# Performance work log

Hardware: AMD Instinct MI355X
Metric: run time of the kernel (lower is better)

Reference implementation:

```python
import jax, jax.numpy as jnp
import numpy as np

OBS, ACT, HID, P, B = 128, 32, 256, 64, 4096
EPS = 1e-5


def _block(x, W, b, g, be, act=True):
    # x: [B, P, Din]; W: [P, Din, Dout]; b/g/be: [P, Dout]
    y = jnp.einsum('bpi,pio->bpo', x, W) + b
    # GroupNorm with one group per sub-policy: normalize over Dout per (b, p)
    mu = jnp.mean(y, axis=-1, keepdims=True)
    var = jnp.var(y, axis=-1, keepdims=True)
    y = (y - mu) * jax.lax.rsqrt(var + EPS) * g + be
    return jax.nn.elu(y) if act else y


def setup_inputs() -> dict:
    key = jax.random.key(0)
    ks = jax.random.split(key, 17)
    s = 0.05
    return {
        'observation': jax.random.normal(ks[0], (B, OBS), dtype=jnp.float32),
        'W1': jax.random.normal(ks[1], (P, OBS, HID), dtype=jnp.float32) * s,
        'b1': jax.random.normal(ks[2], (P, HID), dtype=jnp.float32) * s,
        'g1': jnp.ones((P, HID), dtype=jnp.float32),
        'be1': jnp.zeros((P, HID), dtype=jnp.float32),
        'W2': jax.random.normal(ks[3], (P, HID, HID), dtype=jnp.float32) * s,
        'b2': jax.random.normal(ks[4], (P, HID), dtype=jnp.float32) * s,
        'g2': jnp.ones((P, HID), dtype=jnp.float32),
        'be2': jnp.zeros((P, HID), dtype=jnp.float32),
        'W3': jax.random.normal(ks[5], (P, HID, HID), dtype=jnp.float32) * s,
        'b3': jax.random.normal(ks[6], (P, HID), dtype=jnp.float32) * s,
        'g3': jnp.ones((P, HID), dtype=jnp.float32),
        'be3': jnp.zeros((P, HID), dtype=jnp.float32),
        'W4': jax.random.normal(ks[7], (P, HID, ACT), dtype=jnp.float32) * s,
        'b4': jax.random.normal(ks[8], (P, ACT), dtype=jnp.float32) * s,
        'g4': jnp.ones((P, ACT), dtype=jnp.float32),
        'be4': jnp.zeros((P, ACT), dtype=jnp.float32),
    }


def reference(observation, W1, b1, g1, be1, W2, b2, g2, be2,
              W3, b3, g3, be3, W4, b4, g4, be4):
    # broadcast observation to each sub-policy: [B, P, OBS]
    x = jnp.broadcast_to(observation[:, None, :], (observation.shape[0], P, OBS))
    x = _block(x, W1, b1, g1, be1, act=True)
    x = _block(x, W2, b2, g2, be2, act=True)
    x = _block(x, W3, b3, g3, be3, act=True)
    x = _block(x, W4, b4, g4, be4, act=False)
    return x  # [B, P, ACT] action logits
```

## Files before the change

### kernel.cpp

```cpp
#include <hip/hip_runtime.h>

#define B_    4096
#define P_    64
#define OBS_  128
#define HID_  256
#define ACTD_ 32

typedef __attribute__((ext_vector_type(8)))  __bf16 bf16x8;
typedef __attribute__((ext_vector_type(2)))  __bf16 bf16x2_t;
typedef __attribute__((ext_vector_type(2)))  float  f32x2;
typedef __attribute__((ext_vector_type(4)))  float  f32x4;
typedef __attribute__((ext_vector_type(16))) float  f32x16;

#define XSTRIDE 264

#define WS1 0L
#define WS2 2097152L
#define WS3 6291456L
#define WS4 10485760L

#if defined(__has_builtin)
#if __has_builtin(__builtin_amdgcn_cvt_pk_bf16_f32)
#define HAVE_CVT_PK_BF16 1
#endif
#endif
#ifndef HAVE_CVT_PK_BF16
#define HAVE_CVT_PK_BF16 0
#endif

__device__ __forceinline__ unsigned short f2bf(float x) {
    unsigned u = __builtin_bit_cast(unsigned, x);
    u = (u + 0x7fffu + ((u >> 16) & 1u)) >> 16;
    return (unsigned short)u;
}

__device__ __forceinline__ unsigned pack_bf16_rne(float a, float b) {
#if HAVE_CVT_PK_BF16
    bf16x2_t p = __builtin_amdgcn_cvt_pk_bf16_f32(a, b);
    return __builtin_bit_cast(unsigned, p);
#else
    unsigned ua = __builtin_bit_cast(unsigned, a);
    unsigned ub = __builtin_bit_cast(unsigned, b);
    ua = ua + 0x7fffu + ((ua >> 16) & 1u);
    ub = ub + 0x7fffu + ((ub >> 16) & 1u);
    return __builtin_amdgcn_perm(ub, ua, 0x07060302u);
#endif
}

__device__ __forceinline__ void elu2_asm(float &a, float &b) {
    float ra, rb;
    asm volatile(
        "v_mul_f32 %0, 0x3fb8aa3b, %2\n\t"
        "v_mul_f32 %1, 0x3fb8aa3b, %3\n\t"
        "v_exp_f32 %0, %0\n\t"
        "v_exp_f32 %1, %1\n\t"
        "s_nop 0\n\t"
        "v_add_f32 %0, -1.0, %0\n\t"
        "v_add_f32 %1, -1.0, %1\n\t"
        "v_cmp_lt_f32 vcc, 0, %2\n\t"
        "v_cndmask_b32 %0, %0, %2, vcc\n\t"
        "v_cmp_lt_f32 vcc, 0, %3\n\t"
        "v_cndmask_b32 %1, %1, %3, vcc"
        : "=&v"(ra), "=&v"(rb) : "v"(a), "v"(b) : "vcc");
    a = ra; b = rb;
}

template<int K, int N>
__device__ __forceinline__ void prep_body(const float* __restrict__ W,
                                          unsigned short* __restrict__ out,
                                          int b, int t)
{
    constexpr int CH = K / 32;
    int tid  = b * 256 + t;
    int n    = tid % N;
    int rest = tid / N;
    int u    = rest % 4;
    rest    /= 4;
    int c    = rest % CH;
    int p    = rest / CH;
    const float* __restrict__ src = W + ((long)(p * K + c * 32 + u * 8)) * N + n;
    unsigned short tmp[8];
#pragma unroll
    for (int j = 0; j < 8; ++j)
        tmp[j] = f2bf(src[(long)j * N]);
    unsigned short* dst = out + ((((long)(p * CH + c) * 4 + u) * N + n) * 8);
    *reinterpret_cast<uint4*>(dst) = *reinterpret_cast<const uint4*>(tmp);
}

extern "C" __global__ __launch_bounds__(256)
void prep_all(const float* __restrict__ W1, const float* __restrict__ W2,
              const float* __restrict__ W3, const float* __restrict__ W4,
              unsigned short* __restrict__ ws)
{
    int b = blockIdx.x, t = threadIdx.x;
    if      (b < 1024) prep_body<128, 256>(W1, ws + WS1, b,        t);
    else if (b < 3072) prep_body<256, 256>(W2, ws + WS2, b - 1024, t);
    else if (b < 5120) prep_body<256, 256>(W3, ws + WS3, b - 3072, t);
    else               prep_body<256, 32 >(W4, ws + WS4, b - 5120, t);
}

template<int KCH>
__device__ __forceinline__ void layer256(
    unsigned short* __restrict__ X,
    const char* __restrict__ wsrc,
    const float* __restrict__ bp, const float* __restrict__ gp, const float* __restrict__ bep,
    float2* __restrict__ part, float2* __restrict__ stats,
    int tid, bool elu)
{
    const int w  = tid >> 6;
    const int l5 = tid & 31;
    const int h  = (tid & 63) >> 5;

    const bf16x8* __restrict__ Wp = (const bf16x8*)wsrc + (h * 256 + w * 64 + l5);
    const int nb = w * 64 + 4 * h;

    f32x16 acc[2][2];
#pragma unroll
    for (int nt = 0; nt < 2; ++nt)
#pragma unroll
        for (int q = 0; q < 4; ++q) {
            const float4 b4 = *reinterpret_cast<const float4*>(bp + nb + nt * 32 + 8 * q);
#pragma unroll
            for (int mt = 0; mt < 2; ++mt) {
                acc[nt][mt][4 * q + 0] = b4.x;
                acc[nt][mt][4 * q + 1] = b4.y;
                acc[nt][mt][4 * q + 2] = b4.z;
                acc[nt][mt][4 * q + 3] = b4.w;
            }
        }

    bf16x8 wb0[4], wb1[4];
#pragma unroll
    for (int i = 0; i < 4; ++i) {
        wb0[i] = Wp[i * 512];
        wb1[i] = Wp[i * 512 + 32];
    }
#pragma unroll
    for (int c = 0; c < KCH; ++c) {
        const int k0 = c * 16 + h * 8;
        const bf16x8 w0 = wb0[c & 3];
        const bf16x8 w1 = wb1[c & 3];
        if (c + 4 < KCH) {
            wb0[c & 3] = Wp[(c + 4) * 512];
            wb1[c & 3] = Wp[(c + 4) * 512 + 32];
        }
        bf16x8 x0 = *(const bf16x8*)(X + l5 * XSTRIDE + k0);
        bf16x8 x1 = *(const bf16x8*)(X + (32 + l5) * XSTRIDE + k0);
        acc[0][0] = __builtin_amdgcn_mfma_f32_32x32x16_bf16(w0, x0, acc[0][0], 0, 0, 0);
        acc[0][1] = __builtin_amdgcn_mfma_f32_32x32x16_bf16(w0, x1, acc[0][1], 0, 0, 0);
        acc[1][0] = __builtin_amdgcn_mfma_f32_32x32x16_bf16(w1, x0, acc[1][0], 0, 0, 0);
        acc[1][1] = __builtin_amdgcn_mfma_f32_32x32x16_bf16(w1, x1, acc[1][1], 0, 0, 0);
    }
    __syncthreads();

    {
        f32x2 S0 = {0.f, 0.f}, S20 = {0.f, 0.f};
        f32x2 S1 = {0.f, 0.f}, S21 = {0.f, 0.f};
#pragma unroll
        for (int nt = 0; nt < 2; ++nt)
#pragma unroll
            for (int rp = 0; rp < 8; ++rp) {
                f32x2 v0 = {acc[nt][0][2 * rp], acc[nt][0][2 * rp + 1]};
                f32x2 v1 = {acc[nt][1][2 * rp], acc[nt][1][2 * rp + 1]};
                S0 += v0;  S20 = v0 * v0 + S20;
                S1 += v1;  S21 = v1 * v1 + S21;
            }
        part[l5 * 9 + w * 2 + h]        = make_float2(S0.x + S0.y, S20.x + S20.y);
        part[(32 + l5) * 9 + w * 2 + h] = make_float2(S1.x + S1.y, S21.x + S21.y);
    }
    __syncthreads();
    {
        const int row = tid >> 2, i = tid & 3;
        float2 pa = part[row * 9 + 2 * i];
        float2 pb = part[row * 9 + 2 * i + 1];
        float s  = pa.x + pb.x;
        float s2 = pa.y + pb.y;
        s += __shfl_xor(s, 1);  s2 += __shfl_xor(s2, 1);
        s += __shfl_xor(s, 2);  s2 += __shfl_xor(s2, 2);
        if (i == 0) {
            float mu  = s * (1.f / 256.f);
            float var = s2 * (1.f / 256.f) - mu * mu;
            stats[row] = make_float2(mu, rsqrtf(var + 1e-5f));
        }
    }
    __syncthreads();

    const float2 st0 = stats[l5], st1 = stats[32 + l5];
    const f32x2 mu0v = {st0.x, st0.x}, rs0v = {st0.y, st0.y};
    const f32x2 mu1v = {st1.x, st1.x}, rs1v = {st1.y, st1.y};
#pragma unroll
    for (int nt = 0; nt < 2; ++nt) {
#pragma unroll
        for (int q = 0; q < 4; ++q) {
            const int nq = nb + nt * 32 + 8 * q;
            const float4 g4 = *reinterpret_cast<const float4*>(gp  + nq);
            const float4 e4 = *reinterpret_cast<const float4*>(bep + nq);
            const f32x2 g01 = {g4.x, g4.y}, g23 = {g4.z, g4.w};
            const f32x2 e01 = {e4.x, e4.y}, e23 = {e4.z, e4.w};
#pragma unroll
            for (int mt = 0; mt < 2; ++mt) {
                const f32x2 mu = mt ? mu1v : mu0v;
                const f32x2 rs = mt ? rs1v : rs0v;
                f32x2 y01 = {acc[nt][mt][4 * q + 0], acc[nt][mt][4 * q + 1]};
                f32x2 y23 = {acc[nt][mt][4 * q + 2], acc[nt][mt][4 * q + 3]};
                f32x2 z01 = (y01 - mu) * rs * g01 + e01;
                f32x2 z23 = (y23 - mu) * rs * g23 + e23;
                float v0 = z01.x, v1 = z01.y, v2 = z23.x, v3 = z23.y;
                if (elu) { elu2_asm(v0, v1); elu2_asm(v2, v3); }
                uint2 pk;
                pk.x = pack_bf16_rne(v0, v1);
                pk.y = pack_bf16_rne(v2, v3);
                *reinterpret_cast<uint2*>(X + (mt * 32 + l5) * XSTRIDE + nq) = pk;
            }
        }
    }
    __syncthreads();
}

__device__ __forceinline__ void layer32(
    const unsigned short* __restrict__ X,
    const char* __restrict__ wsrc,
    const float* __restrict__ bp, const float* __restrict__ gp, const float* __restrict__ bep,
    float* __restrict__ outg, int bbase, int p, int tid)
{
    const int w = tid >> 6, lane = tid & 63, ln = lane & 15, quad = lane >> 4;
    const bf16x8* __restrict__ Bp = (const bf16x8*)wsrc + (quad * 32 + ln);

    const float bb0 = bp[ln], bb1 = bp[16 + ln];
    f32x4 acc[2];
#pragma unroll
    for (int r = 0; r < 4; ++r) { acc[0][r] = bb0; acc[1][r] = bb1; }

#pragma unroll
    for (int c = 0; c < 8; ++c) {
        bf16x8 a  = *(const bf16x8*)(X + (16 * w + ln) * XSTRIDE + c * 32 + quad * 8);
        bf16x8 b0 = Bp[c * 128];
        bf16x8 b1 = Bp[c * 128 + 16];
        acc[0] = __builtin_amdgcn_mfma_f32_16x16x32_bf16(a, b0, acc[0], 0, 0, 0);
        acc[1] = __builtin_amdgcn_mfma_f32_16x16x32_bf16(a, b1, acc[1], 0, 0, 0);
    }

    const float g0 = gp[ln], g1 = gp[16 + ln], be0 = bep[ln], be1 = bep[16 + ln];
#pragma unroll
    for (int r = 0; r < 4; ++r) {
        float y0 = acc[0][r], y1 = acc[1][r];
        float s = y0 + y1, s2 = y0 * y0 + y1 * y1;
        s += __shfl_xor(s, 1);  s2 += __shfl_xor(s2, 1);
        s += __shfl_xor(s, 2);  s2 += __shfl_xor(s2, 2);
        s += __shfl_xor(s, 4);  s2 += __shfl_xor(s2, 4);
        s += __shfl_xor(s, 8);  s2 += __shfl_xor(s2, 8);
        float mu  = s * (1.f / 32.f);
        float var = s2 * (1.f / 32.f) - mu * mu;
        float rs  = rsqrtf(var + 1e-5f);
        const int row = bbase + 16 * w + quad * 4 + r;
        float* o = outg + ((long)row * P_ + p) * ACTD_;
        o[ln]      = (y0 - mu) * rs * g0 + be0;
        o[16 + ln] = (y1 - mu) * rs * g1 + be1;
    }
}

extern "C" __global__ void __launch_bounds__(256, 3)
policy_fused(const float* __restrict__ obs,
             const unsigned short* __restrict__ wbf,
             const float* __restrict__ b1, const float* __restrict__ g1, const float* __restrict__ be1,
             const float* __restrict__ b2, const float* __restrict__ g2, const float* __restrict__ be2,
             const float* __restrict__ b3, const float* __restrict__ g3, const float* __restrict__ be3,
             const float* __restrict__ b4, const float* __restrict__ g4, const float* __restrict__ be4,
             float* __restrict__ out)
{
    __shared__ __align__(16) unsigned short X[64 * XSTRIDE];
    __shared__ float2 part[64 * 9];
    __shared__ float2 stats[64];

    const int tid = threadIdx.x;
    const int bx  = blockIdx.x;
    const int p     = ((bx & 7) << 3) | ((bx >> 3) & 7);
    const int bbase = (bx >> 6) * 64;

    const char* ws1 = (const char*)(wbf + WS1 + (long)p * (128 * 256));
    const char* ws2 = (const char*)(wbf + WS2 + (long)p * (256 * 256));
    const char* ws3 = (const char*)(wbf + WS3 + (long)p * (256 * 256));
    const char* ws4 = (const char*)(wbf + WS4 + (long)p * (256 * 32));

    for (int idx = tid; idx < 64 * 32; idx += 256) {
        int row = idx >> 5, c4 = idx & 31;
        float4 v = *reinterpret_cast<const float4*>(obs + (long)(bbase + row) * OBS_ + c4 * 4);
        uint2 pk;
        pk.x = pack_bf16_rne(v.x, v.y);
        pk.y = pack_bf16_rne(v.z, v.w);
        *reinterpret_cast<uint2*>(X + row * XSTRIDE + c4 * 4) = pk;
    }
    __syncthreads();

    layer256<8>(X, ws1, b1 + p * 256, g1 + p * 256, be1 + p * 256, part, stats, tid, true);
    layer256<16>(X, ws2, b2 + p * 256, g2 + p * 256, be2 + p * 256, part, stats, tid, true);
    layer256<16>(X, ws3, b3 + p * 256, g3 + p * 256, be3 + p * 256, part, stats, tid, true);
    layer32(X, ws4, b4 + p * 32, g4 + p * 32, be4 + p * 32, out, bbase, p, tid);
}

extern "C" void kernel_launch(void* const* d_in, const int* in_sizes, int n_in,
                              void* d_out, int out_size, void* d_ws, size_t ws_size,
                              hipStream_t stream)
{
    const float* obs = (const float*)d_in[0];
    const float* W1  = (const float*)d_in[1];
    const float* b1  = (const float*)d_in[2];
    const float* g1  = (const float*)d_in[3];
    const float* be1 = (const float*)d_in[4];
    const float* W2  = (const float*)d_in[5];
    const float* b2  = (const float*)d_in[6];
    const float* g2  = (const float*)d_in[7];
    const float* be2 = (const float*)d_in[8];
    const float* W3  = (const float*)d_in[9];
    const float* b3  = (const float*)d_in[10];
    const float* g3  = (const float*)d_in[11];
    const float* be3 = (const float*)d_in[12];
    const float* W4  = (const float*)d_in[13];
    const float* b4  = (const float*)d_in[14];
    const float* g4  = (const float*)d_in[15];
    const float* be4 = (const float*)d_in[16];
    float* out = (float*)d_out;
    unsigned short* ws = (unsigned short*)d_ws;

    hipLaunchKernelGGL(prep_all, dim3(5376), dim3(256), 0, stream, W1, W2, W3, W4, ws);

    hipLaunchKernelGGL(policy_fused, dim3(4096), dim3(256), 0, stream,
                       obs, ws,
                       b1, g1, be1, b2, g2, be2, b3, g3, be3, b4, g4, be4, out);
}
```

Measured before the change: 268.1 us.

## Outline layer256 into noinline function and raise occupancy to four blocks

```diff
diff --git a/kernel.cpp b/kernel.cpp
--- a/kernel.cpp
+++ b/kernel.cpp
@@ -13,6 +13,11 @@
 typedef __attribute__((ext_vector_type(16))) float  f32x16;
 
 #define XSTRIDE 264
+
+#define X_OFF     0
+#define PART_OFF  33792
+#define STATS_OFF 38400
+#define SMEM_BYTES 38912
 
 #define WS1 0L
 #define WS2 2097152L
@@ -27,6 +32,11 @@
 #ifndef HAVE_CVT_PK_BF16
 #define HAVE_CVT_PK_BF16 0
 #endif
+
+__device__ __forceinline__ unsigned char* smem_base() {
+    extern __shared__ __align__(16) unsigned char smem_dyn[];
+    return smem_dyn;
+}
 
 __device__ __forceinline__ unsigned short f2bf(float x) {
     unsigned u = __builtin_bit_cast(unsigned, x);
@@ -99,14 +109,17 @@
     else               prep_body<256, 32 >(W4, ws + WS4, b - 5120, t);
 }
 
-template<int KCH>
-__device__ __forceinline__ void layer256(
-    unsigned short* __restrict__ X,
+__device__ __attribute__((noinline)) void layer256_fn(
     const char* __restrict__ wsrc,
-    const float* __restrict__ bp, const float* __restrict__ gp, const float* __restrict__ bep,
-    float2* __restrict__ part, float2* __restrict__ stats,
-    int tid, bool elu)
-{
+    const float* __restrict__ bp, const float* __restrict__ gp,
+    const float* __restrict__ bep,
+    int tid, int kch)
+{
+    unsigned char* smem = smem_base();
+    unsigned short* X     = (unsigned short*)(smem + X_OFF);
+    float2*         part  = (float2*)(smem + PART_OFF);
+    float2*         stats = (float2*)(smem + STATS_OFF);
+
     const int w  = tid >> 6;
     const int l5 = tid & 31;
     const int h  = (tid & 63) >> 5;
@@ -129,23 +142,14 @@
             }
         }
 
-    bf16x8 wb0[4], wb1[4];
-#pragma unroll
-    for (int i = 0; i < 4; ++i) {
-        wb0[i] = Wp[i * 512];
-        wb1[i] = Wp[i * 512 + 32];
-    }
-#pragma unroll
-    for (int c = 0; c < KCH; ++c) {
-        const int k0 = c * 16 + h * 8;
-        const bf16x8 w0 = wb0[c & 3];
-        const bf16x8 w1 = wb1[c & 3];
-        if (c + 4 < KCH) {
-            wb0[c & 3] = Wp[(c + 4) * 512];
-            wb1[c & 3] = Wp[(c + 4) * 512 + 32];
-        }
-        bf16x8 x0 = *(const bf16x8*)(X + l5 * XSTRIDE + k0);
-        bf16x8 x1 = *(const bf16x8*)(X + (32 + l5) * XSTRIDE + k0);
+    const unsigned short* __restrict__ Xr0 = X + l5 * XSTRIDE + h * 8;
+    const unsigned short* __restrict__ Xr1 = X + (32 + l5) * XSTRIDE + h * 8;
+#pragma unroll 2
+    for (int c = 0; c < kch; ++c) {
+        bf16x8 x0 = *(const bf16x8*)(Xr0 + c * 16);
+        bf16x8 x1 = *(const bf16x8*)(Xr1 + c * 16);
+        bf16x8 w0 = Wp[c * 512];
+        bf16x8 w1 = Wp[c * 512 + 32];
         acc[0][0] = __builtin_amdgcn_mfma_f32_32x32x16_bf16(w0, x0, acc[0][0], 0, 0, 0);
         acc[0][1] = __builtin_amdgcn_mfma_f32_32x32x16_bf16(w0, x1, acc[0][1], 0, 0, 0);
         acc[1][0] = __builtin_amdgcn_mfma_f32_32x32x16_bf16(w1, x0, acc[1][0], 0, 0, 0);
@@ -206,7 +210,7 @@
                 f32x2 z01 = (y01 - mu) * rs * g01 + e01;
                 f32x2 z23 = (y23 - mu) * rs * g23 + e23;
                 float v0 = z01.x, v1 = z01.y, v2 = z23.x, v3 = z23.y;
-                if (elu) { elu2_asm(v0, v1); elu2_asm(v2, v3); }
+                elu2_asm(v0, v1); elu2_asm(v2, v3);
                 uint2 pk;
                 pk.x = pack_bf16_rne(v0, v1);
                 pk.y = pack_bf16_rne(v2, v3);
@@ -259,7 +263,7 @@
     }
 }
 
-extern "C" __global__ void __launch_bounds__(256, 3)
+extern "C" __global__ void __launch_bounds__(256, 4)
 policy_fused(const float* __restrict__ obs,
              const unsigned short* __restrict__ wbf,
              const float* __restrict__ b1, const float* __restrict__ g1, const float* __restrict__ be1,
@@ -268,9 +272,8 @@
              const float* __restrict__ b4, const float* __restrict__ g4, const float* __restrict__ be4,
              float* __restrict__ out)
 {
-    __shared__ __align__(16) unsigned short X[64 * XSTRIDE];
-    __shared__ float2 part[64 * 9];
-    __shared__ float2 stats[64];
+    unsigned char* smem = smem_base();
+    unsigned short* X = (unsigned short*)(smem + X_OFF);
 
     const int tid = threadIdx.x;
     const int bx  = blockIdx.x;
@@ -292,9 +295,9 @@
     }
     __syncthreads();
 
-    layer256<8>(X, ws1, b1 + p * 256, g1 + p * 256, be1 + p * 256, part, stats, tid, true);
-    layer256<16>(X, ws2, b2 + p * 256, g2 + p * 256, be2 + p * 256, part, stats, tid, true);
-    layer256<16>(X, ws3, b3 + p * 256, g3 + p * 256, be3 + p * 256, part, stats, tid, true);
+    layer256_fn(ws1, b1 + p * 256, g1 + p * 256, be1 + p * 256, tid, 8);
+    layer256_fn(ws2, b2 + p * 256, g2 + p * 256, be2 + p * 256, tid, 16);
+    layer256_fn(ws3, b3 + p * 256, g3 + p * 256, be3 + p * 256, tid, 16);
     layer32(X, ws4, b4 + p * 32, g4 + p * 32, be4 + p * 32, out, bbase, p, tid);
 }
 
@@ -324,7 +327,7 @@
 
     hipLaunchKernelGGL(prep_all, dim3(5376), dim3(256), 0, stream, W1, W2, W3, W4, ws);
 
-    hipLaunchKernelGGL(policy_fused, dim3(4096), dim3(256), 0, stream,
+    hipLaunchKernelGGL(policy_fused, dim3(4096), dim3(256), SMEM_BYTES, stream,
                        obs, ws,
                        b1, g1, be1, b2, g2, be2, b3, g3, be3, b4, g4, be4, out);
 }
```

Measured after the change: 301.0 us. 1.12x slower.
